# Kernel tuning notes

Measured on AMD Instinct MI355X. Metric: run time of the kernel, lower is better.

## Reference

```python
import jax, jax.numpy as jnp
import numpy as np

EPS = 1e-5
NUM_GROUPS = 8


def setup_inputs() -> dict:
    key = jax.random.key(0)
    ks = jax.random.split(key, 7)
    B, C, D, H, W = 2, 128, 16, 16, 16
    s = 1.0 / np.sqrt(C)
    return {
        "x": jax.random.normal(ks[0], (B, C, D, H, W), dtype=jnp.float32),
        "Wq": jax.random.normal(ks[1], (C, C), dtype=jnp.float32) * s,
        "Wk": jax.random.normal(ks[2], (C, C), dtype=jnp.float32) * s,
        "Wv": jax.random.normal(ks[3], (C, C), dtype=jnp.float32) * s,
        "Wo": jax.random.normal(ks[4], (C, C), dtype=jnp.float32) * s,
        "gamma": jnp.ones((C,), dtype=jnp.float32),
        "beta": jnp.zeros((C,), dtype=jnp.float32),
    }


def reference(x, Wq, Wk, Wv, Wo, gamma, beta):
    B, C = x.shape[0], x.shape[1]
    spatial = x.shape[2:]
    xf = x.reshape(B, C, -1)  # [B, C, N]

    # 1x1 conv == channel-mixing matmul
    q = jnp.einsum('oc,bcn->bon', Wq, xf)
    k = jnp.einsum('oc,bcn->bon', Wk, xf)
    v = jnp.einsum('oc,bcn->bon', Wv, xf)

    # unscaled attention: qk[b,n,m] = sum_c q[b,c,n] k[b,c,m]
    w = jax.nn.softmax(jnp.einsum('bcn,bcm->bnm', q, k), axis=-1)  # [B, N, N]
    # h = v @ w^T : h[b,c,n] = sum_m v[b,c,m] w[b,n,m]
    h = jnp.einsum('bcm,bnm->bcn', v, w)
    h = jnp.einsum('oc,bcn->bon', Wo, h)

    y = xf + h
    # GroupNorm(8, C) over (C//G, N) per group
    g = y.reshape(B, NUM_GROUPS, C // NUM_GROUPS, -1)
    mu = jnp.mean(g, axis=(2, 3), keepdims=True)
    var = jnp.mean(jnp.square(g - mu), axis=(2, 3), keepdims=True)
    gn = ((g - mu) * jax.lax.rsqrt(var + EPS)).reshape(B, C, -1)
    out = gn * gamma[None, :, None] + beta[None, :, None]
    out = out * jax.nn.sigmoid(out)  # SiLU
    return out.reshape(B, C, *spatial)
```

## Files before the change

kernel.cpp:

```cpp
#include <hip/hip_runtime.h>

#define CC 128
#define NN 4096
#define NB 2
#define NSPLIT 4
#define TK 64
#define ITERS 16

typedef unsigned short ushort;
typedef unsigned int uint;
typedef __attribute__((ext_vector_type(8))) _Float16 h8;
typedef __attribute__((ext_vector_type(8))) short s8;
typedef __attribute__((ext_vector_type(4))) float f4;
#define MFMA16(a, b, c) __builtin_amdgcn_mfma_f32_16x16x32_f16(a, b, c, 0, 0, 0)
#define MFMAB(a, b, c)  __builtin_amdgcn_mfma_f32_16x16x32_bf16(a, b, c, 0, 0, 0)

__device__ __forceinline__ ushort f2h(float f) {
  _Float16 h = (_Float16)f;
  return *(ushort*)&h;
}
__device__ __forceinline__ ushort f2bf(float f) {
  uint u = __float_as_uint(f);
  u += 0x7fffu + ((u >> 16) & 1u);
  return (ushort)(u >> 16);
}
__device__ __forceinline__ float bf2f(ushort u) {
  return __uint_as_float((uint)u << 16);
}

__global__ __launch_bounds__(256) void qkv_mm(
    const float* __restrict__ x, const float* __restrict__ Wq,
    const float* __restrict__ Wk, const float* __restrict__ Wv,
    ushort* __restrict__ qT, ushort* __restrict__ kT, ushort* __restrict__ vB,
    float* __restrict__ stats) {
  __shared__ ushort Wh[CC][136];
  __shared__ ushort xs[32][136];
  const int t = threadIdx.x;
  const int n0 = blockIdx.x * 32;
  const int b = blockIdx.y;

  if (blockIdx.x == 0 && b == 0 && t < 32) stats[t] = 0.f;

  {
    int c0 = (t & 31) * 4;
    int n4 = (t >> 5) * 4;
    float4 r0 = *(const float4*)&x[((size_t)b * CC + c0 + 0) * NN + n0 + n4];
    float4 r1 = *(const float4*)&x[((size_t)b * CC + c0 + 1) * NN + n0 + n4];
    float4 r2 = *(const float4*)&x[((size_t)b * CC + c0 + 2) * NN + n0 + n4];
    float4 r3 = *(const float4*)&x[((size_t)b * CC + c0 + 3) * NN + n0 + n4];
    ushort4 w0, w1, w2, w3;
    w0.x = f2h(r0.x); w0.y = f2h(r1.x); w0.z = f2h(r2.x); w0.w = f2h(r3.x);
    w1.x = f2h(r0.y); w1.y = f2h(r1.y); w1.z = f2h(r2.y); w1.w = f2h(r3.y);
    w2.x = f2h(r0.z); w2.y = f2h(r1.z); w2.z = f2h(r2.z); w2.w = f2h(r3.z);
    w3.x = f2h(r0.w); w3.y = f2h(r1.w); w3.z = f2h(r2.w); w3.w = f2h(r3.w);
    *(ushort4*)&xs[n4 + 0][c0] = w0;
    *(ushort4*)&xs[n4 + 1][c0] = w1;
    *(ushort4*)&xs[n4 + 2][c0] = w2;
    *(ushort4*)&xs[n4 + 3][c0] = w3;
  }
  __syncthreads();

  const int wv = t >> 6, lane = t & 63;
  const int quad = lane >> 4, l16 = lane & 15;

  for (int which = 0; which < 3; ++which) {
    const float* W = (which == 0) ? Wq : (which == 1) ? Wk : Wv;
#pragma unroll
    for (int i = 0; i < 16; ++i) {
      int slot = t + 256 * i;
      int o = slot >> 5, c4 = (slot & 31) * 4;
      float4 w4 = *(const float4*)&W[o * CC + c4];
      ushort4 p; p.x = f2h(w4.x); p.y = f2h(w4.y); p.z = f2h(w4.z); p.w = f2h(w4.w);
      *(ushort4*)&Wh[o][c4] = p;
    }
    __syncthreads();

    if (which < 2) {
      ushort* out = (which == 0) ? qT : kT;
      f4 acc[2][2];
#pragma unroll
      for (int ot = 0; ot < 2; ++ot)
#pragma unroll
        for (int nt = 0; nt < 2; ++nt) acc[ot][nt] = (f4){0.f, 0.f, 0.f, 0.f};
#pragma unroll
      for (int kk = 0; kk < 4; ++kk) {
        h8 a0 = *(const h8*)&Wh[(wv * 2 + 0) * 16 + l16][kk * 32 + quad * 8];
        h8 a1 = *(const h8*)&Wh[(wv * 2 + 1) * 16 + l16][kk * 32 + quad * 8];
#pragma unroll
        for (int nt = 0; nt < 2; ++nt) {
          h8 bb = *(const h8*)&xs[nt * 16 + l16][kk * 32 + quad * 8];
          acc[0][nt] = MFMA16(a0, bb, acc[0][nt]);
          acc[1][nt] = MFMA16(a1, bb, acc[1][nt]);
        }
      }
#pragma unroll
      for (int ot = 0; ot < 2; ++ot)
#pragma unroll
        for (int nt = 0; nt < 2; ++nt) {
          f4 a = acc[ot][nt];
          ushort4 p; p.x = f2h(a[0]); p.y = f2h(a[1]); p.z = f2h(a[2]); p.w = f2h(a[3]);
          *(ushort4*)&out[((size_t)b * NN + n0 + nt * 16 + l16) * CC +
                          (wv * 2 + ot) * 16 + quad * 4] = p;
        }
    } else {
      f4 acc[2][2];
#pragma unroll
      for (int ci = 0; ci < 2; ++ci)
#pragma unroll
        for (int nt = 0; nt < 2; ++nt) acc[ci][nt] = (f4){0.f, 0.f, 0.f, 0.f};
#pragma unroll
      for (int kk = 0; kk < 4; ++kk) {
        h8 a0 = *(const h8*)&xs[0 * 16 + l16][kk * 32 + quad * 8];
        h8 a1 = *(const h8*)&xs[1 * 16 + l16][kk * 32 + quad * 8];
        h8 b0 = *(const h8*)&Wh[(wv * 2 + 0) * 16 + l16][kk * 32 + quad * 8];
        h8 b1 = *(const h8*)&Wh[(wv * 2 + 1) * 16 + l16][kk * 32 + quad * 8];
        acc[0][0] = MFMA16(a0, b0, acc[0][0]);
        acc[0][1] = MFMA16(a1, b0, acc[0][1]);
        acc[1][0] = MFMA16(a0, b1, acc[1][0]);
        acc[1][1] = MFMA16(a1, b1, acc[1][1]);
      }
#pragma unroll
      for (int ci = 0; ci < 2; ++ci)
#pragma unroll
        for (int nt = 0; nt < 2; ++nt) {
          f4 a = acc[ci][nt];
          ushort4 p; p.x = f2bf(a[0]); p.y = f2bf(a[1]); p.z = f2bf(a[2]); p.w = f2bf(a[3]);
          *(ushort4*)&vB[((size_t)b * CC + (wv * 2 + ci) * 16 + l16) * NN +
                         n0 + nt * 16 + quad * 4] = p;
        }
    }
    __syncthreads();
  }
}

__global__ __launch_bounds__(256) void attn_split(
    const ushort* __restrict__ qTg, const ushort* __restrict__ kTg,
    const ushort* __restrict__ vBg, ushort* __restrict__ Op,
    float* __restrict__ Lg) {
  __shared__ ushort ksT[TK][136];
  __shared__ ushort vs[CC][72];
  __shared__ ushort psb[4][16][72];

  const int t = threadIdx.x;
  const int b = blockIdx.z;
  const int split = blockIdx.y;
  const int n0 = blockIdx.x * 64;
  const int wv = t >> 6;
  const int lane = t & 63;
  const int quad = lane >> 4;
  const int l16 = lane & 15;
  const int nw = n0 + wv * 16;
  const int m00 = split * (NN / NSPLIT);

  const int krow = t >> 4, kcol = (t & 15) * 8;
  const int vrow = t >> 3, vcol = (t & 7) * 8;
  const ushort* kbp = kTg + ((size_t)b * NN + m00 + krow) * CC + kcol;
  const ushort* vbp = vBg + ((size_t)b * CC + vrow) * NN + m00 + vcol;

  const size_t qb = ((size_t)b * NN + nw + l16) * CC + quad * 8;
  h8 aq0 = *(const h8*)&qTg[qb + 0 * 32];
  h8 aq1 = *(const h8*)&qTg[qb + 1 * 32];
  h8 aq2 = *(const h8*)&qTg[qb + 2 * 32];
  h8 aq3 = *(const h8*)&qTg[qb + 3 * 32];

  int4 k0 = *(const int4*)&kbp[0];
  int4 k1 = *(const int4*)&kbp[16 * CC];
  int4 k2 = *(const int4*)&kbp[32 * CC];
  int4 k3 = *(const int4*)&kbp[48 * CC];
  int4 v0 = *(const int4*)&vbp[0];
  int4 v1 = *(const int4*)&vbp[(size_t)32 * NN];
  int4 v2 = *(const int4*)&vbp[(size_t)64 * NN];
  int4 v3 = *(const int4*)&vbp[(size_t)96 * NN];

  s8 ones;
#pragma unroll
  for (int i = 0; i < 8; ++i) ones[i] = (short)0x3F80;

  f4 o0 = {0,0,0,0}, o1 = {0,0,0,0}, o2 = {0,0,0,0}, o3 = {0,0,0,0};
  f4 o4 = {0,0,0,0}, o5 = {0,0,0,0}, o6 = {0,0,0,0}, o7 = {0,0,0,0};
  f4 oL = {0,0,0,0};

  for (int kt = 0; kt < ITERS; ++kt) {
    *(int4*)&ksT[krow][kcol]      = k0;
    *(int4*)&ksT[krow + 16][kcol] = k1;
    *(int4*)&ksT[krow + 32][kcol] = k2;
    *(int4*)&ksT[krow + 48][kcol] = k3;
    *(int4*)&vs[vrow][vcol]       = v0;
    *(int4*)&vs[vrow + 32][vcol]  = v1;
    *(int4*)&vs[vrow + 64][vcol]  = v2;
    *(int4*)&vs[vrow + 96][vcol]  = v3;
    __syncthreads();

    {
      int ktn = (kt + 1 < ITERS) ? kt + 1 : kt;
      const ushort* kp = kbp + (size_t)ktn * TK * CC;
      const ushort* vp = vbp + (size_t)ktn * TK;
      k0 = *(const int4*)&kp[0];
      k1 = *(const int4*)&kp[16 * CC];
      k2 = *(const int4*)&kp[32 * CC];
      k3 = *(const int4*)&kp[48 * CC];
      v0 = *(const int4*)&vp[0];
      v1 = *(const int4*)&vp[(size_t)32 * NN];
      v2 = *(const int4*)&vp[(size_t)64 * NN];
      v3 = *(const int4*)&vp[(size_t)96 * NN];
    }

    f4 s0 = {0,0,0,0}, s1 = {0,0,0,0}, s2 = {0,0,0,0}, s3 = {0,0,0,0};
#pragma unroll
    for (int kk = 0; kk < 4; ++kk) {
      h8 a = (kk == 0) ? aq0 : (kk == 1) ? aq1 : (kk == 2) ? aq2 : aq3;
      h8 b0 = *(const h8*)&ksT[l16][kk * 32 + quad * 8];
      h8 b1 = *(const h8*)&ksT[16 + l16][kk * 32 + quad * 8];
      h8 b2 = *(const h8*)&ksT[32 + l16][kk * 32 + quad * 8];
      h8 b3 = *(const h8*)&ksT[48 + l16][kk * 32 + quad * 8];
      s0 = MFMA16(b0, a, s0);
      s1 = MFMA16(b1, a, s1);
      s2 = MFMA16(b2, a, s2);
      s3 = MFMA16(b3, a, s3);
    }

    {
      ushort4 pk;
      pk.x = f2bf(__expf(s0[0])); pk.y = f2bf(__expf(s0[1]));
      pk.z = f2bf(__expf(s0[2])); pk.w = f2bf(__expf(s0[3]));
      *(ushort4*)&psb[wv][l16][0 + quad * 4] = pk;
      pk.x = f2bf(__expf(s1[0])); pk.y = f2bf(__expf(s1[1]));
      pk.z = f2bf(__expf(s1[2])); pk.w = f2bf(__expf(s1[3]));
      *(ushort4*)&psb[wv][l16][16 + quad * 4] = pk;
      pk.x = f2bf(__expf(s2[0])); pk.y = f2bf(__expf(s2[1]));
      pk.z = f2bf(__expf(s2[2])); pk.w = f2bf(__expf(s2[3]));
      *(ushort4*)&psb[wv][l16][32 + quad * 4] = pk;
      pk.x = f2bf(__expf(s3[0])); pk.y = f2bf(__expf(s3[1]));
      pk.z = f2bf(__expf(s3[2])); pk.w = f2bf(__expf(s3[3]));
      *(ushort4*)&psb[wv][l16][48 + quad * 4] = pk;
    }

#pragma unroll
    for (int mk = 0; mk < 2; ++mk) {
      s8 bp = *(const s8*)&psb[wv][l16][mk * 32 + quad * 8];
      s8 a0 = *(const s8*)&vs[0 * 16 + l16][mk * 32 + quad * 8];
      s8 a1 = *(const s8*)&vs[1 * 16 + l16][mk * 32 + quad * 8];
      s8 a2 = *(const s8*)&vs[2 * 16 + l16][mk * 32 + quad * 8];
      s8 a3 = *(const s8*)&vs[3 * 16 + l16][mk * 32 + quad * 8];
      o0 = MFMAB(a0, bp, o0);
      o1 = MFMAB(a1, bp, o1);
      o2 = MFMAB(a2, bp, o2);
      o3 = MFMAB(a3, bp, o3);
      s8 a4 = *(const s8*)&vs[4 * 16 + l16][mk * 32 + quad * 8];
      s8 a5 = *(const s8*)&vs[5 * 16 + l16][mk * 32 + quad * 8];
      s8 a6 = *(const s8*)&vs[6 * 16 + l16][mk * 32 + quad * 8];
      s8 a7 = *(const s8*)&vs[7 * 16 + l16][mk * 32 + quad * 8];
      o4 = MFMAB(a4, bp, o4);
      o5 = MFMAB(a5, bp, o5);
      o6 = MFMAB(a6, bp, o6);
      o7 = MFMAB(a7, bp, o7);
      oL = MFMAB(ones, bp, oL);
    }
    __syncthreads();
  }

  if (quad == 0)
    Lg[((size_t)(split * NB + b)) * NN + nw + l16] = oL[0];
  {
    size_t nb_ = ((size_t)(split * NB + b) * NN + nw + l16) * CC + quad * 4;
    ushort4 p;
#define STORE_O(oo, off) \
    p.x = f2bf(oo[0]); p.y = f2bf(oo[1]); p.z = f2bf(oo[2]); p.w = f2bf(oo[3]); \
    *(ushort4*)&Op[nb_ + off] = p;
    STORE_O(o0, 0 * 16) STORE_O(o1, 1 * 16) STORE_O(o2, 2 * 16) STORE_O(o3, 3 * 16)
    STORE_O(o4, 4 * 16) STORE_O(o5, 5 * 16) STORE_O(o6, 6 * 16) STORE_O(o7, 7 * 16)
#undef STORE_O
  }
}

__global__ __launch_bounds__(256) void proj_mm(
    const float* __restrict__ x, const float* __restrict__ Wo,
    const ushort* __restrict__ Op, const float* __restrict__ Lg,
    float* __restrict__ y, float* __restrict__ stats) {
  __shared__ ushort Wh[CC][136];
  __shared__ ushort hT[32][136];
  __shared__ float Linv[32];
  const int t = threadIdx.x;
  const int n0 = blockIdx.x * 32;
  const int b = blockIdx.y;

#pragma unroll
  for (int i = 0; i < 16; ++i) {
    int slot = t + 256 * i;
    int o = slot >> 5, c4 = (slot & 31) * 4;
    float4 w4 = *(const float4*)&Wo[o * CC + c4];
    ushort4 p; p.x = f2h(w4.x); p.y = f2h(w4.y); p.z = f2h(w4.z); p.w = f2h(w4.w);
    *(ushort4*)&Wh[o][c4] = p;
  }
  if (t < 32) {
    float l = 0.f;
#pragma unroll
    for (int s = 0; s < NSPLIT; ++s)
      l += Lg[(size_t)(s * NB + b) * NN + n0 + t];
    Linv[t] = 1.f / l;
  }
  __syncthreads();

#pragma unroll
  for (int i = 0; i < 16; ++i) {
    int slot = t + 256 * i;
    int n = slot >> 5, c4 = (slot & 31) * 4;
    size_t base = ((size_t)(n0 + n)) * CC + c4;
    float a0 = 0.f, a1 = 0.f, a2 = 0.f, a3 = 0.f;
#pragma unroll
    for (int s = 0; s < NSPLIT; ++s) {
      ushort4 u = *(const ushort4*)&Op[(size_t)(s * NB + b) * NN * CC + base];
      a0 += bf2f(u.x); a1 += bf2f(u.y); a2 += bf2f(u.z); a3 += bf2f(u.w);
    }
    float li = Linv[n];
    ushort4 p;
    p.x = f2h(a0 * li); p.y = f2h(a1 * li);
    p.z = f2h(a2 * li); p.w = f2h(a3 * li);
    *(ushort4*)&hT[n][c4] = p;
  }
  __syncthreads();

  const int wv = t >> 6, lane = t & 63;
  const int quad = lane >> 4, l16 = lane & 15;

  f4 acc[2][2];
#pragma unroll
  for (int nt = 0; nt < 2; ++nt)
#pragma unroll
    for (int ot = 0; ot < 2; ++ot) acc[nt][ot] = (f4){0.f, 0.f, 0.f, 0.f};
#pragma unroll
  for (int kk = 0; kk < 4; ++kk) {
    h8 a0 = *(const h8*)&hT[0 * 16 + l16][kk * 32 + quad * 8];
    h8 a1 = *(const h8*)&hT[1 * 16 + l16][kk * 32 + quad * 8];
    h8 b0 = *(const h8*)&Wh[(wv * 2 + 0) * 16 + l16][kk * 32 + quad * 8];
    h8 b1 = *(const h8*)&Wh[(wv * 2 + 1) * 16 + l16][kk * 32 + quad * 8];
    acc[0][0] = MFMA16(a0, b0, acc[0][0]);
    acc[0][1] = MFMA16(a0, b1, acc[0][1]);
    acc[1][0] = MFMA16(a1, b0, acc[1][0]);
    acc[1][1] = MFMA16(a1, b1, acc[1][1]);
  }

#pragma unroll
  for (int ot = 0; ot < 2; ++ot) {
    const int o = (wv * 2 + ot) * 16 + l16;
    const int g = wv * 2 + ot;
    float s = 0.f, sq = 0.f;
#pragma unroll
    for (int nt = 0; nt < 2; ++nt) {
      size_t addr = ((size_t)b * CC + o) * NN + n0 + nt * 16 + quad * 4;
      float4 xv = *(const float4*)&x[addr];
      f4 a = acc[nt][ot];
      float4 yy;
      yy.x = a[0] + xv.x; yy.y = a[1] + xv.y;
      yy.z = a[2] + xv.z; yy.w = a[3] + xv.w;
      *(float4*)&y[addr] = yy;
      s += yy.x + yy.y + yy.z + yy.w;
      sq += yy.x * yy.x + yy.y * yy.y + yy.z * yy.z + yy.w * yy.w;
    }
#pragma unroll
    for (int off = 1; off < 64; off <<= 1) {
      s += __shfl_xor(s, off);
      sq += __shfl_xor(sq, off);
    }
    if (lane == 0) {
      atomicAdd(&stats[(b * 8 + g) * 2 + 0], s);
      atomicAdd(&stats[(b * 8 + g) * 2 + 1], sq);
    }
  }
}

__global__ __launch_bounds__(256) void gn_silu(
    const float* __restrict__ y, const float* __restrict__ stats,
    const float* __restrict__ gamma, const float* __restrict__ beta,
    float* __restrict__ out) {
  const int tid = blockIdx.x * 256 + threadIdx.x;
  const int i4 = tid * 4;
  const int c = (i4 >> 12) & (CC - 1);
  const int b = i4 >> 19;
  const int g = c >> 4;
  const float inv = 1.f / 65536.f;
  float sum = stats[(b * 8 + g) * 2 + 0];
  float sq  = stats[(b * 8 + g) * 2 + 1];
  float mean = sum * inv;
  float var = sq * inv - mean * mean;
  float rs = rsqrtf(var + 1e-5f);
  float ga = gamma[c], be = beta[c];
  float4 v4 = *(const float4*)&y[i4];
  float4 r;
  float o;
  o = (v4.x - mean) * rs * ga + be; r.x = o / (1.f + __expf(-o));
  o = (v4.y - mean) * rs * ga + be; r.y = o / (1.f + __expf(-o));
  o = (v4.z - mean) * rs * ga + be; r.z = o / (1.f + __expf(-o));
  o = (v4.w - mean) * rs * ga + be; r.w = o / (1.f + __expf(-o));
  *(float4*)&out[i4] = r;
}

extern "C" void kernel_launch(void* const* d_in, const int* in_sizes, int n_in,
                              void* d_out, int out_size, void* d_ws, size_t ws_size,
                              hipStream_t stream) {
  const float* x     = (const float*)d_in[0];
  const float* Wq    = (const float*)d_in[1];
  const float* Wk    = (const float*)d_in[2];
  const float* Wv    = (const float*)d_in[3];
  const float* Wo    = (const float*)d_in[4];
  const float* gamma = (const float*)d_in[5];
  const float* beta  = (const float*)d_in[6];
  float* out = (float*)d_out;
  float* ws  = (float*)d_ws;

  const size_t M = (size_t)NB * CC * NN;
  ushort* Op = (ushort*)ws;
  ushort* qT = (ushort*)(ws + 2 * M);
  ushort* kT = qT + M;
  float* y = ws + 2 * M;
  ushort* vB = kT + M;
  float* Lg = (float*)(vB + M);
  float* stats = Lg + (size_t)NSPLIT * NB * NN;

  qkv_mm<<<dim3(NN / 32, NB), 256, 0, stream>>>(x, Wq, Wk, Wv, qT, kT, vB, stats);
  attn_split<<<dim3(NN / 64, NSPLIT, NB), 256, 0, stream>>>(qT, kT, vB, Op, Lg);
  proj_mm<<<dim3(NN / 32, NB), 256, 0, stream>>>(x, Wo, Op, Lg, y, stats);
  gn_silu<<<dim3((int)(M / 1024)), 256, 0, stream>>>(y, stats, gamma, beta, out);
}
```

Before: 147.7 us.

## Double per-wave query tile in attention and load weights directly from global

Each attention wave now computes two 16-row query tiles against the same staged K/V tiles, halving the grid and the K/V LDS traffic per query row. The qkv and output projection kernels drop the LDS weight staging and the barriers around it, loading fp32 weight fragments directly from global memory and converting them to fp16 in registers. The costs are more accumulator registers in attention, lower block count and occupancy, and redundant global weight reads that rely on cache hits.

```diff
diff --git a/kernel.cpp b/kernel.cpp
--- a/kernel.cpp
+++ b/kernel.cpp
@@ -28,12 +28,22 @@
   return __uint_as_float((uint)u << 16);
 }
 
+__device__ __forceinline__ h8 ldw8(const float* __restrict__ W, int row, int col) {
+  float4 f0 = *(const float4*)&W[row * CC + col];
+  float4 f1 = *(const float4*)&W[row * CC + col + 4];
+  h8 r;
+  r[0] = (_Float16)f0.x; r[1] = (_Float16)f0.y;
+  r[2] = (_Float16)f0.z; r[3] = (_Float16)f0.w;
+  r[4] = (_Float16)f1.x; r[5] = (_Float16)f1.y;
+  r[6] = (_Float16)f1.z; r[7] = (_Float16)f1.w;
+  return r;
+}
+
 __global__ __launch_bounds__(256) void qkv_mm(
     const float* __restrict__ x, const float* __restrict__ Wq,
     const float* __restrict__ Wk, const float* __restrict__ Wv,
     ushort* __restrict__ qT, ushort* __restrict__ kT, ushort* __restrict__ vB,
     float* __restrict__ stats) {
-  __shared__ ushort Wh[CC][136];
   __shared__ ushort xs[32][136];
   const int t = threadIdx.x;
   const int n0 = blockIdx.x * 32;
@@ -62,74 +72,66 @@
 
   const int wv = t >> 6, lane = t & 63;
   const int quad = lane >> 4, l16 = lane & 15;
-
-  for (int which = 0; which < 3; ++which) {
-    const float* W = (which == 0) ? Wq : (which == 1) ? Wk : Wv;
-#pragma unroll
-    for (int i = 0; i < 16; ++i) {
-      int slot = t + 256 * i;
-      int o = slot >> 5, c4 = (slot & 31) * 4;
-      float4 w4 = *(const float4*)&W[o * CC + c4];
-      ushort4 p; p.x = f2h(w4.x); p.y = f2h(w4.y); p.z = f2h(w4.z); p.w = f2h(w4.w);
-      *(ushort4*)&Wh[o][c4] = p;
-    }
-    __syncthreads();
-
-    if (which < 2) {
-      ushort* out = (which == 0) ? qT : kT;
-      f4 acc[2][2];
-#pragma unroll
-      for (int ot = 0; ot < 2; ++ot)
-#pragma unroll
-        for (int nt = 0; nt < 2; ++nt) acc[ot][nt] = (f4){0.f, 0.f, 0.f, 0.f};
-#pragma unroll
-      for (int kk = 0; kk < 4; ++kk) {
-        h8 a0 = *(const h8*)&Wh[(wv * 2 + 0) * 16 + l16][kk * 32 + quad * 8];
-        h8 a1 = *(const h8*)&Wh[(wv * 2 + 1) * 16 + l16][kk * 32 + quad * 8];
-#pragma unroll
-        for (int nt = 0; nt < 2; ++nt) {
-          h8 bb = *(const h8*)&xs[nt * 16 + l16][kk * 32 + quad * 8];
-          acc[0][nt] = MFMA16(a0, bb, acc[0][nt]);
-          acc[1][nt] = MFMA16(a1, bb, acc[1][nt]);
-        }
-      }
-#pragma unroll
-      for (int ot = 0; ot < 2; ++ot)
-#pragma unroll
-        for (int nt = 0; nt < 2; ++nt) {
-          f4 a = acc[ot][nt];
-          ushort4 p; p.x = f2h(a[0]); p.y = f2h(a[1]); p.z = f2h(a[2]); p.w = f2h(a[3]);
-          *(ushort4*)&out[((size_t)b * NN + n0 + nt * 16 + l16) * CC +
-                          (wv * 2 + ot) * 16 + quad * 4] = p;
-        }
-    } else {
-      f4 acc[2][2];
-#pragma unroll
-      for (int ci = 0; ci < 2; ++ci)
-#pragma unroll
-        for (int nt = 0; nt < 2; ++nt) acc[ci][nt] = (f4){0.f, 0.f, 0.f, 0.f};
-#pragma unroll
-      for (int kk = 0; kk < 4; ++kk) {
-        h8 a0 = *(const h8*)&xs[0 * 16 + l16][kk * 32 + quad * 8];
-        h8 a1 = *(const h8*)&xs[1 * 16 + l16][kk * 32 + quad * 8];
-        h8 b0 = *(const h8*)&Wh[(wv * 2 + 0) * 16 + l16][kk * 32 + quad * 8];
-        h8 b1 = *(const h8*)&Wh[(wv * 2 + 1) * 16 + l16][kk * 32 + quad * 8];
-        acc[0][0] = MFMA16(a0, b0, acc[0][0]);
-        acc[0][1] = MFMA16(a1, b0, acc[0][1]);
-        acc[1][0] = MFMA16(a0, b1, acc[1][0]);
-        acc[1][1] = MFMA16(a1, b1, acc[1][1]);
-      }
-#pragma unroll
-      for (int ci = 0; ci < 2; ++ci)
-#pragma unroll
-        for (int nt = 0; nt < 2; ++nt) {
-          f4 a = acc[ci][nt];
-          ushort4 p; p.x = f2bf(a[0]); p.y = f2bf(a[1]); p.z = f2bf(a[2]); p.w = f2bf(a[3]);
-          *(ushort4*)&vB[((size_t)b * CC + (wv * 2 + ci) * 16 + l16) * NN +
-                         n0 + nt * 16 + quad * 4] = p;
-        }
-    }
-    __syncthreads();
+  const int r0 = (wv * 2 + 0) * 16 + l16;
+  const int r1 = (wv * 2 + 1) * 16 + l16;
+
+#pragma unroll
+  for (int which = 0; which < 2; ++which) {
+    const float* W = which ? Wk : Wq;
+    ushort* out = which ? kT : qT;
+    f4 acc[2][2];
+#pragma unroll
+    for (int ot = 0; ot < 2; ++ot)
+#pragma unroll
+      for (int nt = 0; nt < 2; ++nt) acc[ot][nt] = (f4){0.f, 0.f, 0.f, 0.f};
+#pragma unroll
+    for (int kk = 0; kk < 4; ++kk) {
+      h8 a0 = ldw8(W, r0, kk * 32 + quad * 8);
+      h8 a1 = ldw8(W, r1, kk * 32 + quad * 8);
+#pragma unroll
+      for (int nt = 0; nt < 2; ++nt) {
+        h8 bb = *(const h8*)&xs[nt * 16 + l16][kk * 32 + quad * 8];
+        acc[0][nt] = MFMA16(a0, bb, acc[0][nt]);
+        acc[1][nt] = MFMA16(a1, bb, acc[1][nt]);
+      }
+    }
+#pragma unroll
+    for (int ot = 0; ot < 2; ++ot)
+#pragma unroll
+      for (int nt = 0; nt < 2; ++nt) {
+        f4 a = acc[ot][nt];
+        ushort4 p; p.x = f2h(a[0]); p.y = f2h(a[1]); p.z = f2h(a[2]); p.w = f2h(a[3]);
+        *(ushort4*)&out[((size_t)b * NN + n0 + nt * 16 + l16) * CC +
+                        (wv * 2 + ot) * 16 + quad * 4] = p;
+      }
+  }
+
+  {
+    f4 acc[2][2];
+#pragma unroll
+    for (int ci = 0; ci < 2; ++ci)
+#pragma unroll
+      for (int nt = 0; nt < 2; ++nt) acc[ci][nt] = (f4){0.f, 0.f, 0.f, 0.f};
+#pragma unroll
+    for (int kk = 0; kk < 4; ++kk) {
+      h8 a0 = *(const h8*)&xs[0 * 16 + l16][kk * 32 + quad * 8];
+      h8 a1 = *(const h8*)&xs[1 * 16 + l16][kk * 32 + quad * 8];
+      h8 b0 = ldw8(Wv, r0, kk * 32 + quad * 8);
+      h8 b1 = ldw8(Wv, r1, kk * 32 + quad * 8);
+      acc[0][0] = MFMA16(a0, b0, acc[0][0]);
+      acc[0][1] = MFMA16(a1, b0, acc[0][1]);
+      acc[1][0] = MFMA16(a0, b1, acc[1][0]);
+      acc[1][1] = MFMA16(a1, b1, acc[1][1]);
+    }
+#pragma unroll
+    for (int ci = 0; ci < 2; ++ci)
+#pragma unroll
+      for (int nt = 0; nt < 2; ++nt) {
+        f4 a = acc[ci][nt];
+        ushort4 p; p.x = f2bf(a[0]); p.y = f2bf(a[1]); p.z = f2bf(a[2]); p.w = f2bf(a[3]);
+        *(ushort4*)&vB[((size_t)b * CC + (wv * 2 + ci) * 16 + l16) * NN +
+                       n0 + nt * 16 + quad * 4] = p;
+      }
   }
 }
 
@@ -139,17 +141,17 @@
     float* __restrict__ Lg) {
   __shared__ ushort ksT[TK][136];
   __shared__ ushort vs[CC][72];
-  __shared__ ushort psb[4][16][72];
+  __shared__ ushort psb[4][32][72];
 
   const int t = threadIdx.x;
   const int b = blockIdx.z;
   const int split = blockIdx.y;
-  const int n0 = blockIdx.x * 64;
+  const int n0 = blockIdx.x * 128;
   const int wv = t >> 6;
   const int lane = t & 63;
   const int quad = lane >> 4;
   const int l16 = lane & 15;
-  const int nw = n0 + wv * 16;
+  const int nw = n0 + wv * 32;
   const int m00 = split * (NN / NSPLIT);
 
   const int krow = t >> 4, kcol = (t & 15) * 8;
@@ -157,11 +159,14 @@
   const ushort* kbp = kTg + ((size_t)b * NN + m00 + krow) * CC + kcol;
   const ushort* vbp = vBg + ((size_t)b * CC + vrow) * NN + m00 + vcol;
 
-  const size_t qb = ((size_t)b * NN + nw + l16) * CC + quad * 8;
-  h8 aq0 = *(const h8*)&qTg[qb + 0 * 32];
-  h8 aq1 = *(const h8*)&qTg[qb + 1 * 32];
-  h8 aq2 = *(const h8*)&qTg[qb + 2 * 32];
-  h8 aq3 = *(const h8*)&qTg[qb + 3 * 32];
+  const size_t qb0 = ((size_t)b * NN + nw + l16) * CC + quad * 8;
+  const size_t qb1 = qb0 + (size_t)16 * CC;
+  h8 aq[2][4];
+#pragma unroll
+  for (int kk = 0; kk < 4; ++kk) {
+    aq[0][kk] = *(const h8*)&qTg[qb0 + kk * 32];
+    aq[1][kk] = *(const h8*)&qTg[qb1 + kk * 32];
+  }
 
   int4 k0 = *(const int4*)&kbp[0];
   int4 k1 = *(const int4*)&kbp[16 * CC];
@@ -176,9 +181,14 @@
 #pragma unroll
   for (int i = 0; i < 8; ++i) ones[i] = (short)0x3F80;
 
-  f4 o0 = {0,0,0,0}, o1 = {0,0,0,0}, o2 = {0,0,0,0}, o3 = {0,0,0,0};
-  f4 o4 = {0,0,0,0}, o5 = {0,0,0,0}, o6 = {0,0,0,0}, o7 = {0,0,0,0};
-  f4 oL = {0,0,0,0};
+  f4 o[2][8];
+#pragma unroll
+  for (int j = 0; j < 2; ++j)
+#pragma unroll
+    for (int ct = 0; ct < 8; ++ct) o[j][ct] = (f4){0.f, 0.f, 0.f, 0.f};
+  f4 oL[2];
+  oL[0] = (f4){0.f, 0.f, 0.f, 0.f};
+  oL[1] = (f4){0.f, 0.f, 0.f, 0.f};
 
   for (int kt = 0; kt < ITERS; ++kt) {
     *(int4*)&ksT[krow][kcol]      = k0;
@@ -205,71 +215,66 @@
       v3 = *(const int4*)&vp[(size_t)96 * NN];
     }
 
-    f4 s0 = {0,0,0,0}, s1 = {0,0,0,0}, s2 = {0,0,0,0}, s3 = {0,0,0,0};
+    f4 s[2][4];
+#pragma unroll
+    for (int j = 0; j < 2; ++j)
+#pragma unroll
+      for (int mt = 0; mt < 4; ++mt) s[j][mt] = (f4){0.f, 0.f, 0.f, 0.f};
 #pragma unroll
     for (int kk = 0; kk < 4; ++kk) {
-      h8 a = (kk == 0) ? aq0 : (kk == 1) ? aq1 : (kk == 2) ? aq2 : aq3;
-      h8 b0 = *(const h8*)&ksT[l16][kk * 32 + quad * 8];
+      h8 b0 = *(const h8*)&ksT[ 0 + l16][kk * 32 + quad * 8];
       h8 b1 = *(const h8*)&ksT[16 + l16][kk * 32 + quad * 8];
       h8 b2 = *(const h8*)&ksT[32 + l16][kk * 32 + quad * 8];
       h8 b3 = *(const h8*)&ksT[48 + l16][kk * 32 + quad * 8];
-      s0 = MFMA16(b0, a, s0);
-      s1 = MFMA16(b1, a, s1);
-      s2 = MFMA16(b2, a, s2);
-      s3 = MFMA16(b3, a, s3);
-    }
-
-    {
-      ushort4 pk;
-      pk.x = f2bf(__expf(s0[0])); pk.y = f2bf(__expf(s0[1]));
-      pk.z = f2bf(__expf(s0[2])); pk.w = f2bf(__expf(s0[3]));
-      *(ushort4*)&psb[wv][l16][0 + quad * 4] = pk;
-      pk.x = f2bf(__expf(s1[0])); pk.y = f2bf(__expf(s1[1]));
-      pk.z = f2bf(__expf(s1[2])); pk.w = f2bf(__expf(s1[3]));
-      *(ushort4*)&psb[wv][l16][16 + quad * 4] = pk;
-      pk.x = f2bf(__expf(s2[0])); pk.y = f2bf(__expf(s2[1]));
-      pk.z = f2bf(__expf(s2[2])); pk.w = f2bf(__expf(s2[3]));
-      *(ushort4*)&psb[wv][l16][32 + quad * 4] = pk;
-      pk.x = f2bf(__expf(s3[0])); pk.y = f2bf(__expf(s3[1]));
-      pk.z = f2bf(__expf(s3[2])); pk.w = f2bf(__expf(s3[3]));
-      *(ushort4*)&psb[wv][l16][48 + quad * 4] = pk;
-    }
+#pragma unroll
+      for (int j = 0; j < 2; ++j) {
+        s[j][0] = MFMA16(b0, aq[j][kk], s[j][0]);
+        s[j][1] = MFMA16(b1, aq[j][kk], s[j][1]);
+        s[j][2] = MFMA16(b2, aq[j][kk], s[j][2]);
+        s[j][3] = MFMA16(b3, aq[j][kk], s[j][3]);
+      }
+    }
+
+#pragma unroll
+    for (int j = 0; j < 2; ++j)
+#pragma unroll
+      for (int mt = 0; mt < 4; ++mt) {
+        ushort4 pk;
+        pk.x = f2bf(__expf(s[j][mt][0]));
+        pk.y = f2bf(__expf(s[j][mt][1]));
+        pk.z = f2bf(__expf(s[j][mt][2]));
+        pk.w = f2bf(__expf(s[j][mt][3]));
+        *(ushort4*)&psb[wv][j * 16 + l16][mt * 16 + quad * 4] = pk;
+      }
 
 #pragma unroll
     for (int mk = 0; mk < 2; ++mk) {
-      s8 bp = *(const s8*)&psb[wv][l16][mk * 32 + quad * 8];
-      s8 a0 = *(const s8*)&vs[0 * 16 + l16][mk * 32 + quad * 8];
-      s8 a1 = *(const s8*)&vs[1 * 16 + l16][mk * 32 + quad * 8];
-      s8 a2 = *(const s8*)&vs[2 * 16 + l16][mk * 32 + quad * 8];
-      s8 a3 = *(const s8*)&vs[3 * 16 + l16][mk * 32 + quad * 8];
-      o0 = MFMAB(a0, bp, o0);
-      o1 = MFMAB(a1, bp, o1);
-      o2 = MFMAB(a2, bp, o2);
-      o3 = MFMAB(a3, bp, o3);
-      s8 a4 = *(const s8*)&vs[4 * 16 + l16][mk * 32 + quad * 8];
-      s8 a5 = *(const s8*)&vs[5 * 16 + l16][mk * 32 + quad * 8];
-      s8 a6 = *(const s8*)&vs[6 * 16 + l16][mk * 32 + quad * 8];
-      s8 a7 = *(const s8*)&vs[7 * 16 + l16][mk * 32 + quad * 8];
-      o4 = MFMAB(a4, bp, o4);
-      o5 = MFMAB(a5, bp, o5);
-      o6 = MFMAB(a6, bp, o6);
-      o7 = MFMAB(a7, bp, o7);
-      oL = MFMAB(ones, bp, oL);
+      s8 bp0 = *(const s8*)&psb[wv][ 0 + l16][mk * 32 + quad * 8];
+      s8 bp1 = *(const s8*)&psb[wv][16 + l16][mk * 32 + quad * 8];
+#pragma unroll
+      for (int ct = 0; ct < 8; ++ct) {
+        s8 a = *(const s8*)&vs[ct * 16 + l16][mk * 32 + quad * 8];
+        o[0][ct] = MFMAB(a, bp0, o[0][ct]);
+        o[1][ct] = MFMAB(a, bp1, o[1][ct]);
+      }
+      oL[0] = MFMAB(ones, bp0, oL[0]);
+      oL[1] = MFMAB(ones, bp1, oL[1]);
     }
     __syncthreads();
   }
 
-  if (quad == 0)
-    Lg[((size_t)(split * NB + b)) * NN + nw + l16] = oL[0];
-  {
-    size_t nb_ = ((size_t)(split * NB + b) * NN + nw + l16) * CC + quad * 4;
+#pragma unroll
+  for (int j = 0; j < 2; ++j) {
+    if (quad == 0)
+      Lg[((size_t)(split * NB + b)) * NN + nw + j * 16 + l16] = oL[j][0];
+    size_t nb_ = ((size_t)(split * NB + b) * NN + nw + j * 16 + l16) * CC + quad * 4;
     ushort4 p;
-#define STORE_O(oo, off) \
-    p.x = f2bf(oo[0]); p.y = f2bf(oo[1]); p.z = f2bf(oo[2]); p.w = f2bf(oo[3]); \
-    *(ushort4*)&Op[nb_ + off] = p;
-    STORE_O(o0, 0 * 16) STORE_O(o1, 1 * 16) STORE_O(o2, 2 * 16) STORE_O(o3, 3 * 16)
-    STORE_O(o4, 4 * 16) STORE_O(o5, 5 * 16) STORE_O(o6, 6 * 16) STORE_O(o7, 7 * 16)
-#undef STORE_O
+#pragma unroll
+    for (int ct = 0; ct < 8; ++ct) {
+      f4 a = o[j][ct];
+      p.x = f2bf(a[0]); p.y = f2bf(a[1]); p.z = f2bf(a[2]); p.w = f2bf(a[3]);
+      *(ushort4*)&Op[nb_ + ct * 16] = p;
+    }
   }
 }
 
@@ -277,21 +282,12 @@
     const float* __restrict__ x, const float* __restrict__ Wo,
     const ushort* __restrict__ Op, const float* __restrict__ Lg,
     float* __restrict__ y, float* __restrict__ stats) {
-  __shared__ ushort Wh[CC][136];
   __shared__ ushort hT[32][136];
   __shared__ float Linv[32];
   const int t = threadIdx.x;
   const int n0 = blockIdx.x * 32;
   const int b = blockIdx.y;
 
-#pragma unroll
-  for (int i = 0; i < 16; ++i) {
-    int slot = t + 256 * i;
-    int o = slot >> 5, c4 = (slot & 31) * 4;
-    float4 w4 = *(const float4*)&Wo[o * CC + c4];
-    ushort4 p; p.x = f2h(w4.x); p.y = f2h(w4.y); p.z = f2h(w4.z); p.w = f2h(w4.w);
-    *(ushort4*)&Wh[o][c4] = p;
-  }
   if (t < 32) {
     float l = 0.f;
 #pragma unroll
@@ -322,6 +318,8 @@
 
   const int wv = t >> 6, lane = t & 63;
   const int quad = lane >> 4, l16 = lane & 15;
+  const int r0 = (wv * 2 + 0) * 16 + l16;
+  const int r1 = (wv * 2 + 1) * 16 + l16;
 
   f4 acc[2][2];
 #pragma unroll
@@ -332,8 +330,8 @@
   for (int kk = 0; kk < 4; ++kk) {
     h8 a0 = *(const h8*)&hT[0 * 16 + l16][kk * 32 + quad * 8];
     h8 a1 = *(const h8*)&hT[1 * 16 + l16][kk * 32 + quad * 8];
-    h8 b0 = *(const h8*)&Wh[(wv * 2 + 0) * 16 + l16][kk * 32 + quad * 8];
-    h8 b1 = *(const h8*)&Wh[(wv * 2 + 1) * 16 + l16][kk * 32 + quad * 8];
+    h8 b0 = ldw8(Wo, r0, kk * 32 + quad * 8);
+    h8 b1 = ldw8(Wo, r1, kk * 32 + quad * 8);
     acc[0][0] = MFMA16(a0, b0, acc[0][0]);
     acc[0][1] = MFMA16(a0, b1, acc[0][1]);
     acc[1][0] = MFMA16(a1, b0, acc[1][0]);
@@ -418,7 +416,7 @@
   float* stats = Lg + (size_t)NSPLIT * NB * NN;
 
   qkv_mm<<<dim3(NN / 32, NB), 256, 0, stream>>>(x, Wq, Wk, Wv, qT, kT, vB, stats);
-  attn_split<<<dim3(NN / 64, NSPLIT, NB), 256, 0, stream>>>(qT, kT, vB, Op, Lg);
+  attn_split<<<dim3(NN / 128, NSPLIT, NB), 256, 0, stream>>>(qT, kT, vB, Op, Lg);
   proj_mm<<<dim3(NN / 32, NB), 256, 0, stream>>>(x, Wo, Op, Lg, y, stats);
   gn_silu<<<dim3((int)(M / 1024)), 256, 0, stream>>>(y, stats, gamma, beta, out);
 }
```

Result: slower. 154.3 us (+4.5%).
